# Optimization experiments

Measured on AMD Instinct MI355X. Metric: run time of the kernel, lower is better.

## Reference

```python
import jax, jax.numpy as jnp
import numpy as np

B, T, C, H = 2, 2048, 2048, 16
HD = C // H  # head_dim = 128


def setup_inputs() -> dict:
    key = jax.random.key(0)
    k1, k2, k3 = jax.random.split(key, 3)
    x = jax.random.normal(k1, (B, T, C), dtype=jnp.float32)
    # causal mask: positions with mask==0 are blocked (masked_fill(mask==0, -inf))
    mask = jnp.tril(jnp.ones((T, T), dtype=bool))[None, None]  # [1,1,T,T]
    W_qkv = jax.random.normal(k2, (C, 3 * C), dtype=jnp.float32) * (C ** -0.5)
    W_proj = jax.random.normal(k3, (C, C), dtype=jnp.float32) * (C ** -0.5)
    b_proj = jnp.zeros((C,), dtype=jnp.float32)
    return {"x": x, "mask": mask, "W_qkv": W_qkv, "W_proj": W_proj, "b_proj": b_proj}


def reference(x, mask, W_qkv, W_proj, b_proj):
    # QKV projection (Linear, bias=False)
    qkv = jnp.einsum('btc,cd->btd', x, W_qkv)            # [B,T,3C]
    qkv = qkv.reshape(B, T, 3, H, HD)
    q = qkv[:, :, 0].transpose(0, 2, 1, 3)               # [B,H,T,HD]
    k = qkv[:, :, 1].transpose(0, 2, 1, 3)
    v = qkv[:, :, 2].transpose(0, 2, 1, 3)
    # scaled dot-product attention (dropout is identity in eval)
    att = jnp.einsum('bhqd,bhkd->bhqk', q, k) / jnp.sqrt(jnp.float32(HD))
    att = jnp.where(mask, att, -jnp.inf)
    att = jax.nn.softmax(att, axis=-1)
    y = jnp.einsum('bhqk,bhkd->bhqd', att, v)            # [B,H,T,HD]
    y = y.transpose(0, 2, 1, 3).reshape(B, T, C)
    return jnp.einsum('btc,cd->btd', y, W_proj) + b_proj
```

## Files before the change

kernel.cpp:

```cpp
#include <hip/hip_runtime.h>
#include <hip/hip_bf16.h>

#define B_  2
#define T_  2048
#define C_  2048
#define H_  16
#define HD_ 128

using bf16x8 = __attribute__((ext_vector_type(8))) __bf16;
using f32x4  = __attribute__((ext_vector_type(4))) float;

__device__ __forceinline__ unsigned short f2bs(float f) {
    __hip_bfloat16 h = __float2bfloat16(f);
    return __builtin_bit_cast(unsigned short, h);
}

__device__ __forceinline__ void gload_lds16(const unsigned short* g, unsigned short* l) {
    __builtin_amdgcn_global_load_lds(
        (const __attribute__((address_space(1))) unsigned int*)g,
        (__attribute__((address_space(3))) unsigned int*)l, 16, 0, 0);
}

__global__ __launch_bounds__(256) void k_prep(const float* __restrict__ x,
                                              unsigned short* __restrict__ XB,
                                              const float* __restrict__ Wqkv,
                                              unsigned short* __restrict__ WQKVT,
                                              const float* __restrict__ Wproj,
                                              unsigned short* __restrict__ WPROJT) {
    __shared__ unsigned short t[64][65];
    int blk = blockIdx.x;
    int tid = threadIdx.x;
    if (blk < 8192) {
        int i = blk * 256 + tid;
        float4 v = reinterpret_cast<const float4*>(x)[i];
        ushort4 o;
        o.x = f2bs(v.x); o.y = f2bs(v.y); o.z = f2bs(v.z); o.w = f2bs(v.w);
        reinterpret_cast<ushort4*>(XB)[i] = o;
        return;
    }
    const float* in;
    unsigned short* out;
    int K = 2048, N, bx, by;
    if (blk < 11264) {
        in = Wqkv; out = WQKVT; N = 6144;
        bx = (blk - 8192) % 96; by = (blk - 8192) / 96;
    } else {
        in = Wproj; out = WPROJT; N = 2048;
        bx = (blk - 11264) % 32; by = (blk - 11264) / 32;
    }
    int k0 = by * 64, n0 = bx * 64;
#pragma unroll
    for (int p = 0; p < 4; ++p) {
        int idx = p * 256 + tid;
        int r = idx >> 4, c = (idx & 15) << 2;
        float4 v = *reinterpret_cast<const float4*>(in + (long)(k0 + r) * N + n0 + c);
        t[r][c] = f2bs(v.x); t[r][c + 1] = f2bs(v.y);
        t[r][c + 2] = f2bs(v.z); t[r][c + 3] = f2bs(v.w);
    }
    __syncthreads();
#pragma unroll
    for (int p = 0; p < 4; ++p) {
        int idx = p * 256 + tid;
        int r = idx >> 4, c = (idx & 15) << 2;
        ushort4 o;
        o.x = t[c][r]; o.y = t[c + 1][r]; o.z = t[c + 2][r]; o.w = t[c + 3][r];
        *reinterpret_cast<ushort4*>(out + (long)(n0 + r) * K + k0 + c) = o;
    }
}

template <int MODE>
__global__ __launch_bounds__(256, 2) void k_gemm(const unsigned short* __restrict__ A,
                                                 const unsigned short* __restrict__ Bt,
                                                 int M, int N, int K,
                                                 unsigned short* __restrict__ qkv,
                                                 float* __restrict__ out,
                                                 const float* __restrict__ bias) {
    __shared__ __align__(16) unsigned short lA[2][128 * 32];
    __shared__ __align__(16) unsigned short lB[2][128 * 32];

    int tid = threadIdx.x;
    int wave = tid >> 6, lane = tid & 63;
    int quad = lane >> 4, l16 = lane & 15;
    int wr = (wave >> 1) * 64, wc = (wave & 1) * 64;
    int m0 = blockIdx.y * 128, n0 = blockIdx.x * 128;

    int lrow = lane >> 2;
    int lcol = (lane & 3) << 3;
    const unsigned short* gA0 = A + (long)(m0 + wave * 32 + lrow) * K + lcol;
    const unsigned short* gA1 = A + (long)(m0 + wave * 32 + 16 + lrow) * K + lcol;
    const unsigned short* gB0 = Bt + (long)(n0 + wave * 32 + lrow) * K + lcol;
    const unsigned short* gB1 = Bt + (long)(n0 + wave * 32 + 16 + lrow) * K + lcol;
    int lofs0 = wave * 1024, lofs1 = wave * 1024 + 512;

    f32x4 zero = {0.f, 0.f, 0.f, 0.f};
    f32x4 acc[4][4];
#pragma unroll
    for (int i = 0; i < 4; ++i)
#pragma unroll
        for (int j = 0; j < 4; ++j) acc[i][j] = zero;

    for (int k0 = 0; k0 < K; k0 += 64) {
        __syncthreads();
#pragma unroll
        for (int h = 0; h < 2; ++h) {
            int kk = k0 + h * 32;
            gload_lds16(gA0 + kk, &lA[h][lofs0]);
            gload_lds16(gA1 + kk, &lA[h][lofs1]);
            gload_lds16(gB0 + kk, &lB[h][lofs0]);
            gload_lds16(gB1 + kk, &lB[h][lofs1]);
        }
        __syncthreads();
#pragma unroll
        for (int h = 0; h < 2; ++h) {
            bf16x8 af[4], bfr[4];
#pragma unroll
            for (int i = 0; i < 4; ++i)
                af[i] = *reinterpret_cast<const bf16x8*>(&lA[h][(wr + i * 16 + l16) * 32 + quad * 8]);
#pragma unroll
            for (int j = 0; j < 4; ++j)
                bfr[j] = *reinterpret_cast<const bf16x8*>(&lB[h][(wc + j * 16 + l16) * 32 + quad * 8]);
#pragma unroll
            for (int i = 0; i < 4; ++i)
#pragma unroll
                for (int j = 0; j < 4; ++j)
                    acc[i][j] = __builtin_amdgcn_mfma_f32_16x16x32_bf16(af[i], bfr[j], acc[i][j], 0, 0, 0);
        }
    }

#pragma unroll
    for (int i = 0; i < 4; ++i) {
#pragma unroll
        for (int j = 0; j < 4; ++j) {
#pragma unroll
            for (int r = 0; r < 4; ++r) {
                int m = m0 + wr + i * 16 + quad * 4 + r;
                int n = n0 + wc + j * 16 + l16;
                float v = acc[i][j][r];
                if (MODE == 0) {
                    int s = n >> 11, col = n & 2047;
                    int h = col >> 7, hd = col & 127;
                    int b = m >> 11, t = m & 2047;
                    long base = (long)s * (B_ * H_ * T_ * HD_);
                    if (s == 2)
                        qkv[base + ((long)(b * H_ + h) * HD_ + hd) * T_ + t] = f2bs(v);
                    else
                        qkv[base + ((long)(b * H_ + h) * T_ + t) * HD_ + hd] = f2bs(v);
                } else {
                    out[(long)m * N + n] = v + bias[n];
                }
            }
        }
    }
}

__global__ __launch_bounds__(256, 3) void k_attn(const unsigned short* __restrict__ qkv,
                                                 unsigned short* __restrict__ y) {
    __shared__ __align__(16) unsigned short lK[64 * 136];
    __shared__ __align__(16) unsigned short lVt[128 * 72];
    __shared__ __align__(16) unsigned short lP[4][16 * 72];

    int tid = threadIdx.x;
    int wave = tid >> 6, lane = tid & 63;
    int quad = lane >> 4, l16 = lane & 15;
    int bh = blockIdx.x;
    int qb = ((int)gridDim.y - 1 - (int)blockIdx.y) * 64;

    const unsigned short* Qh = qkv + (long)bh * (T_ * HD_);
    const unsigned short* Kh = qkv + (long)(B_ * H_) * T_ * HD_ + (long)bh * (T_ * HD_);
    const unsigned short* Vt = qkv + 2L * (B_ * H_) * T_ * HD_ + (long)bh * (HD_ * T_);

    bf16x8 aQ[4];
    int qrow = qb + wave * 16 + l16;
#pragma unroll
    for (int kk = 0; kk < 4; ++kk)
        aQ[kk] = *reinterpret_cast<const bf16x8*>(Qh + (long)qrow * HD_ + kk * 32 + quad * 8);

    float m_s[4], l_s[4];
    f32x4 O[8];
    f32x4 zero = {0.f, 0.f, 0.f, 0.f};
#pragma unroll
    for (int r = 0; r < 4; ++r) { m_s[r] = -1e30f; l_s[r] = 0.f; }
#pragma unroll
    for (int h = 0; h < 8; ++h) O[h] = zero;

    int qmax = qb + wave * 16 + 15;
    const float scl = 0.08838834764831845f;

    for (int kb = 0; kb < qb + 64; kb += 64) {
        __syncthreads();
#pragma unroll
        for (int p = 0; p < 4; ++p) {
            int id = p * 256 + tid;
            int r = id >> 4, cc = (id & 15) << 3;
            *reinterpret_cast<int4*>(&lK[r * 136 + cc]) =
                *reinterpret_cast<const int4*>(Kh + (long)(kb + r) * HD_ + cc);
        }
#pragma unroll
        for (int p = 0; p < 4; ++p) {
            int id = p * 256 + tid;
            int r = id >> 3, cc = (id & 7) << 3;
            *reinterpret_cast<int4*>(&lVt[r * 72 + cc]) =
                *reinterpret_cast<const int4*>(Vt + (long)r * T_ + kb + cc);
        }
        __syncthreads();
        if (kb > qmax) continue;

        f32x4 s[4];
#pragma unroll
        for (int st = 0; st < 4; ++st) s[st] = zero;
#pragma unroll
        for (int kk = 0; kk < 4; ++kk) {
#pragma unroll
            for (int st = 0; st < 4; ++st) {
                bf16x8 b = *reinterpret_cast<const bf16x8*>(
                    &lK[(st * 16 + l16) * 136 + kk * 32 + quad * 8]);
                s[st] = __builtin_amdgcn_mfma_f32_16x16x32_bf16(aQ[kk], b, s[st], 0, 0, 0);
            }
        }

        int qg = qb + wave * 16 + quad * 4;
#pragma unroll
        for (int r = 0; r < 4; ++r) {
            int q = qg + r;
            float x[4];
#pragma unroll
            for (int st = 0; st < 4; ++st)
                x[st] = (kb + st * 16 + l16 <= q) ? s[st][r] * scl : -1e30f;
            float mx = fmaxf(fmaxf(x[0], x[1]), fmaxf(x[2], x[3]));
#pragma unroll
            for (int off = 1; off < 16; off <<= 1) mx = fmaxf(mx, __shfl_xor(mx, off));
            float mn = fmaxf(m_s[r], mx);
            float al = __expf(m_s[r] - mn);
            float p[4], rs = 0.f;
#pragma unroll
            for (int st = 0; st < 4; ++st) { p[st] = __expf(x[st] - mn); rs += p[st]; }
#pragma unroll
            for (int off = 1; off < 16; off <<= 1) rs += __shfl_xor(rs, off);
            m_s[r] = mn;
            l_s[r] = l_s[r] * al + rs;
            int row = quad * 4 + r;
#pragma unroll
            for (int st = 0; st < 4; ++st)
                lP[wave][row * 72 + st * 16 + l16] = f2bs(p[st]);
#pragma unroll
            for (int h = 0; h < 8; ++h) O[h][r] *= al;
        }

#pragma unroll
        for (int kc = 0; kc < 2; ++kc) {
            bf16x8 pf = *reinterpret_cast<const bf16x8*>(
                &lP[wave][l16 * 72 + kc * 32 + quad * 8]);
#pragma unroll
            for (int h = 0; h < 8; ++h) {
                bf16x8 vf = *reinterpret_cast<const bf16x8*>(
                    &lVt[(h * 16 + l16) * 72 + kc * 32 + quad * 8]);
                O[h] = __builtin_amdgcn_mfma_f32_16x16x32_bf16(pf, vf, O[h], 0, 0, 0);
            }
        }
    }

    int b = bh >> 4, hh = bh & 15;
#pragma unroll
    for (int r = 0; r < 4; ++r) {
        int t = qb + wave * 16 + quad * 4 + r;
        float inv = 1.f / l_s[r];
#pragma unroll
        for (int h = 0; h < 8; ++h)
            y[(long)(b * T_ + t) * C_ + hh * HD_ + h * 16 + l16] = f2bs(O[h][r] * inv);
    }
}

extern "C" void kernel_launch(void* const* d_in, const int* in_sizes, int n_in,
                              void* d_out, int out_size, void* d_ws, size_t ws_size,
                              hipStream_t stream) {
    const float* x     = (const float*)d_in[0];
    const float* Wqkv  = (const float*)d_in[2];
    const float* Wproj = (const float*)d_in[3];
    const float* bproj = (const float*)d_in[4];
    float* out = (float*)d_out;

    unsigned short* XB     = (unsigned short*)d_ws;
    unsigned short* WQKVT  = XB + 8388608;
    unsigned short* WPROJT = WQKVT + 12582912;
    unsigned short* QKV    = WPROJT + 4194304;
    if (ws_size < 100663296) return;

    k_prep<<<12288, 256, 0, stream>>>(x, XB, Wqkv, WQKVT, Wproj, WPROJT);
    k_gemm<0><<<dim3(6144 / 128, 4096 / 128), 256, 0, stream>>>(XB, WQKVT, 4096, 6144, 2048,
                                                                QKV, nullptr, nullptr);
    k_attn<<<dim3(32, 32), 256, 0, stream>>>(QKV, XB);
    k_gemm<1><<<dim3(2048 / 128, 4096 / 128), 256, 0, stream>>>(XB, WPROJT, 4096, 2048, 2048,
                                                                nullptr, out, bproj);
}
```

Measured before the change: 404.9 us.

## Load K/V tiles via global_load_lds and use exp2 softmax with deferred row-sum reduction

The attention kernel now stages K and V^T tiles into LDS with direct global-to-LDS 16-byte loads, using a split per-32-column layout instead of padded register-staged copies. This removes the VGPR round trip and spare instructions in the load phase. The softmax folds log2(e) into the scale and uses exp2f, and the per-lane partial row sums are reduced across lanes only once at the end instead of every iteration. The unpadded 32-element LDS rows may cause more bank conflicts on the MFMA operand reads.

```diff
diff --git a/kernel.cpp b/kernel.cpp
--- a/kernel.cpp
+++ b/kernel.cpp
@@ -155,8 +155,8 @@
 
 __global__ __launch_bounds__(256, 3) void k_attn(const unsigned short* __restrict__ qkv,
                                                  unsigned short* __restrict__ y) {
-    __shared__ __align__(16) unsigned short lK[64 * 136];
-    __shared__ __align__(16) unsigned short lVt[128 * 72];
+    __shared__ __align__(16) unsigned short lK[4][64 * 32];
+    __shared__ __align__(16) unsigned short lVt[2][128 * 32];
     __shared__ __align__(16) unsigned short lP[4][16 * 72];
 
     int tid = threadIdx.x;
@@ -175,6 +175,10 @@
     for (int kk = 0; kk < 4; ++kk)
         aQ[kk] = *reinterpret_cast<const bf16x8*>(Qh + (long)qrow * HD_ + kk * 32 + quad * 8);
 
+    int lrow = lane >> 2, lcol = (lane & 3) << 3;
+    const unsigned short* gK = Kh + (long)(wave * 16 + lrow) * HD_ + lcol;
+    const unsigned short* gV = Vt + (long)(wave * 32 + lrow) * T_ + lcol;
+
     float m_s[4], l_s[4];
     f32x4 O[8];
     f32x4 zero = {0.f, 0.f, 0.f, 0.f};
@@ -184,23 +188,17 @@
     for (int h = 0; h < 8; ++h) O[h] = zero;
 
     int qmax = qb + wave * 16 + 15;
-    const float scl = 0.08838834764831845f;
+    const float scl2 = 0.1275174365f;
 
     for (int kb = 0; kb < qb + 64; kb += 64) {
         __syncthreads();
 #pragma unroll
-        for (int p = 0; p < 4; ++p) {
-            int id = p * 256 + tid;
-            int r = id >> 4, cc = (id & 15) << 3;
-            *reinterpret_cast<int4*>(&lK[r * 136 + cc]) =
-                *reinterpret_cast<const int4*>(Kh + (long)(kb + r) * HD_ + cc);
-        }
-#pragma unroll
-        for (int p = 0; p < 4; ++p) {
-            int id = p * 256 + tid;
-            int r = id >> 3, cc = (id & 7) << 3;
-            *reinterpret_cast<int4*>(&lVt[r * 72 + cc]) =
-                *reinterpret_cast<const int4*>(Vt + (long)r * T_ + kb + cc);
+        for (int kk = 0; kk < 4; ++kk)
+            gload_lds16(gK + kb * HD_ + kk * 32, &lK[kk][wave * 512]);
+#pragma unroll
+        for (int kc = 0; kc < 2; ++kc) {
+            gload_lds16(gV + kb + kc * 32, &lVt[kc][wave * 1024]);
+            gload_lds16(gV + 16 * T_ + kb + kc * 32, &lVt[kc][wave * 1024 + 512]);
         }
         __syncthreads();
         if (kb > qmax) continue;
@@ -213,7 +211,7 @@
 #pragma unroll
             for (int st = 0; st < 4; ++st) {
                 bf16x8 b = *reinterpret_cast<const bf16x8*>(
-                    &lK[(st * 16 + l16) * 136 + kk * 32 + quad * 8]);
+                    &lK[kk][(st * 16 + l16) * 32 + quad * 8]);
                 s[st] = __builtin_amdgcn_mfma_f32_16x16x32_bf16(aQ[kk], b, s[st], 0, 0, 0);
             }
         }
@@ -225,19 +223,17 @@
             float x[4];
 #pragma unroll
             for (int st = 0; st < 4; ++st)
-                x[st] = (kb + st * 16 + l16 <= q) ? s[st][r] * scl : -1e30f;
+                x[st] = (kb + st * 16 + l16 <= q) ? s[st][r] * scl2 : -1e30f;
             float mx = fmaxf(fmaxf(x[0], x[1]), fmaxf(x[2], x[3]));
 #pragma unroll
             for (int off = 1; off < 16; off <<= 1) mx = fmaxf(mx, __shfl_xor(mx, off));
             float mn = fmaxf(m_s[r], mx);
-            float al = __expf(m_s[r] - mn);
-            float p[4], rs = 0.f;
-#pragma unroll
-            for (int st = 0; st < 4; ++st) { p[st] = __expf(x[st] - mn); rs += p[st]; }
-#pragma unroll
-            for (int off = 1; off < 16; off <<= 1) rs += __shfl_xor(rs, off);
+            float al = exp2f(m_s[r] - mn);
+            float p[4], ps = 0.f;
+#pragma unroll
+            for (int st = 0; st < 4; ++st) { p[st] = exp2f(x[st] - mn); ps += p[st]; }
             m_s[r] = mn;
-            l_s[r] = l_s[r] * al + rs;
+            l_s[r] = l_s[r] * al + ps;
             int row = quad * 4 + r;
 #pragma unroll
             for (int st = 0; st < 4; ++st)
@@ -253,7 +249,7 @@
 #pragma unroll
             for (int h = 0; h < 8; ++h) {
                 bf16x8 vf = *reinterpret_cast<const bf16x8*>(
-                    &lVt[(h * 16 + l16) * 72 + kc * 32 + quad * 8]);
+                    &lVt[kc][(h * 16 + l16) * 32 + quad * 8]);
                 O[h] = __builtin_amdgcn_mfma_f32_16x16x32_bf16(pf, vf, O[h], 0, 0, 0);
             }
         }
@@ -262,8 +258,11 @@
     int b = bh >> 4, hh = bh & 15;
 #pragma unroll
     for (int r = 0; r < 4; ++r) {
+        float l = l_s[r];
+#pragma unroll
+        for (int off = 1; off < 16; off <<= 1) l += __shfl_xor(l, off);
+        float inv = 1.f / l;
         int t = qb + wave * 16 + quad * 4 + r;
-        float inv = 1.f / l_s[r];
 #pragma unroll
         for (int h = 0; h < 8; ++h)
             y[(long)(b * T_ + t) * C_ + hh * HD_ + h * 16 + l16] = f2bs(O[h][r] * inv);
```

New measurement: 405.2 us. No clear change (+0.1%).
